# Performance work log

Measured on AMD Instinct MI355X. Metric: run time of the kernel, lower is better.

## Reference

```python
import jax, jax.numpy as jnp
import numpy as np

P, Q = 5, 4
C_IN, C_OUT = 256, 256


def setup_inputs() -> dict:
    key = jax.random.key(0)
    kx, kwp, kbp, kwq = jax.random.split(key, 4)
    x = jax.random.normal(kx, (32, C_IN, 56, 56), dtype=jnp.float32)
    # 1x1 conv weights: convp_i -> Wp[i-1] of shape [O, C]; only convp_1 has bias.
    Wp = jax.random.normal(kwp, (P, C_OUT, C_IN), dtype=jnp.float32) * (1.0 / np.sqrt(C_IN))
    bp = jax.random.normal(kbp, (C_OUT,), dtype=jnp.float32) * 0.01
    Wq = jax.random.normal(kwq, (Q, C_OUT, C_IN), dtype=jnp.float32) * (1.0 / np.sqrt(C_IN))
    return {"x": x, "Wp": Wp, "bp": bp, "Wq": Wq}


def reference(x, Wp, bp, Wq):
    # Build powers x**1 .. x**max(P,Q) via incremental multiply (same math as x**i).
    pmax = max(P, Q)
    pows = [x]
    for _ in range(pmax - 1):
        pows.append(pows[-1] * x)
    Xs = jnp.stack(pows, axis=0)  # [pmax, B, C, H, W]
    # Each 1x1 conv is a pointwise channel-mixing GEMM; sum over orders p/q.
    sum_p = jnp.einsum('pbchw,poc->bohw', Xs[:P], Wp) + bp[None, :, None, None]
    sum_q = jnp.einsum('qbchw,qoc->bohw', Xs[:Q], Wq)
    return sum_p / (1.0 + jnp.abs(sum_q))
```

## Files before the change

### kernel.cpp

```cpp
#include <hip/hip_runtime.h>


typedef __attribute__((ext_vector_type(8))) short bf16x8;
typedef __attribute__((ext_vector_type(4))) float f32x4;

#define CIN    256
#define HW3    3136
#define MTOT   100352
#define KTOT   1280
#define WPLANE (512 * 1280)

__device__ __forceinline__ unsigned short f2bf(float f) {
    union { float f; unsigned int u; } cv; cv.f = f;
    unsigned int u = cv.u;
    return (unsigned short)((u + 0x7FFFu + ((u >> 16) & 1u)) >> 16);
}
__device__ __forceinline__ float bf2f(unsigned short h) {
    union { unsigned int u; float f; } cv; cv.u = ((unsigned int)h) << 16;
    return cv.f;
}

__global__ void pack_w_kernel(const float* __restrict__ Wp,
                              const float* __restrict__ Wq,
                              unsigned short* __restrict__ Whi,
                              unsigned short* __restrict__ Wlo) {
    int idx = blockIdx.x * 256 + threadIdx.x;
    int n = idx / KTOT;
    int k = idx - n * KTOT;
    int p = k >> 8, c = k & 255;
    int o = ((n >> 5) << 4) + (n & 15);
    int isq = (n >> 4) & 1;
    float v;
    if (isq) v = (p < 4) ? Wq[((size_t)p * 256 + o) * 256 + c] : 0.0f;
    else     v = Wp[((size_t)p * 256 + o) * 256 + c];
    unsigned short h = f2bf(v);
    Whi[idx] = h;
    Wlo[idx] = f2bf(v - bf2f(h));
}

__device__ __forceinline__ bf16x8 pack_hi8(const float* v) {
    const unsigned int* u = (const unsigned int*)v;
    union { unsigned int w[4]; bf16x8 h; } r;
    r.w[0] = __builtin_amdgcn_perm(u[1], u[0], 0x07060302);
    r.w[1] = __builtin_amdgcn_perm(u[3], u[2], 0x07060302);
    r.w[2] = __builtin_amdgcn_perm(u[5], u[4], 0x07060302);
    r.w[3] = __builtin_amdgcn_perm(u[7], u[6], 0x07060302);
    return r.h;
}
__device__ __forceinline__ void resid8(const float* v, float* l) {
#pragma unroll
    for (int j = 0; j < 8; ++j) {
        union { unsigned int u; float f; } cv;
        cv.u = ((const unsigned int*)v)[j] & 0xFFFF0000u;
        l[j] = v[j] - cv.f;
    }
}

__global__ __launch_bounds__(256, 2) void kanv_gemm(
    const float* __restrict__ x,
    const unsigned short* __restrict__ Whi,
    const unsigned short* __restrict__ Wlo,
    const float* __restrict__ bp,
    float* __restrict__ out)
{
    __shared__ __align__(16) char sB[8 * 8192];

    const int tid  = threadIdx.x;
    const int lane = tid & 63;
    const int wave = tid >> 6;
    const int wm   = wave >> 1;
    const int wn   = wave & 1;
    const int col  = lane & 15;
    const int quad = lane >> 4;

    const int nt = blockIdx.x & 3;
    const int mt = blockIdx.x >> 2;
    const int m0 = mt * 128 + wm * 64;

    const float* xb[4];
#pragma unroll
    for (int mi = 0; mi < 4; ++mi) {
        int m  = m0 + mi * 16 + col;
        int bb = m / HW3, hw = m - bb * HW3;
        xb[mi] = x + ((size_t)bb * CIN) * HW3 + hw;
    }
    const unsigned short* wl4[2];
#pragma unroll
    for (int e = 0; e < 2; ++e) {
        int n = nt * 128 + wn * 64 + (2 * e) * 16 + col;
        wl4[e] = Wlo + (size_t)n * KTOT + quad * 8 + 4 * 256;
    }

    int voff[2];
#pragma unroll
    for (int ii = 0; ii < 2; ++ii) {
        int i = wave + 4 * ii;
        int n = i * 16 + col;
        voff[ii] = (nt * 128 + n) * 2560 + quad * 16;
    }
    const int rbase = (wn * 4) * 1024 + quad * 256 + col * 16;

    f32x4 acc[4][4];
#pragma unroll
    for (int mi = 0; mi < 4; ++mi)
#pragma unroll
        for (int ni = 0; ni < 4; ++ni)
            acc[mi][ni] = (f32x4){0.f, 0.f, 0.f, 0.f};

    float xv[4][8], pw[4][8], xn[4][8];

#pragma unroll
    for (int mi = 0; mi < 4; ++mi) {
        const float* xp = xb[mi] + (size_t)(quad * 8) * HW3;
#pragma unroll
        for (int j = 0; j < 8; ++j) { xv[mi][j] = xp[(size_t)j * HW3]; pw[mi][j] = xv[mi][j]; }
    }

    for (int g = 0; g < 8; ++g) {
        __syncthreads();

#pragma unroll
        for (int s = 0; s < 8; ++s) {
            const unsigned short* plane = (s < 5) ? Whi : Wlo;
            const int p = (s < 5) ? s : (s - 4);
            const char* srcb = (const char*)plane + (size_t)((p * 256 + g * 32) * 2);
#pragma unroll
            for (int ii = 0; ii < 2; ++ii) {
                const int i = wave + 4 * ii;
                __builtin_amdgcn_global_load_lds(
                    (const __attribute__((address_space(1))) void*)(srcb + voff[ii]),
                    (__attribute__((address_space(3))) void*)(sB + s * 8192 + i * 1024),
                    16, 0, 0);
            }
        }
        __syncthreads();

        if (g < 7) {
#pragma unroll
            for (int mi = 0; mi < 4; ++mi) {
                const float* xp = xb[mi] + (size_t)((g + 1) * 32 + quad * 8) * HW3;
#pragma unroll
                for (int j = 0; j < 8; ++j) xn[mi][j] = xp[(size_t)j * HW3];
            }
        }

#pragma unroll
        for (int p = 0; p < 5; ++p) {
            bf16x8 ah[4], al[4];
#pragma unroll
            for (int mi = 0; mi < 4; ++mi) {
                ah[mi] = pack_hi8(pw[mi]);
                if (p > 0) {
                    float lo[8];
                    resid8(pw[mi], lo);
                    al[mi] = pack_hi8(lo);
                }
            }
            const char* sb_p = sB + p * 8192 + rbase;
#pragma unroll
            for (int ni = 0; ni < 4; ++ni) {
                if (p == 4 && (ni & 1)) continue;
                bf16x8 bh = *(const bf16x8*)(sb_p + ni * 1024);
#pragma unroll
                for (int mi = 0; mi < 4; ++mi)
                    acc[mi][ni] = __builtin_amdgcn_mfma_f32_16x16x32_bf16(ah[mi], bh, acc[mi][ni], 0, 0, 0);
                if (p > 0) {
                    bf16x8 bl;
                    if (p < 4) bl = *(const bf16x8*)(sB + (p + 4) * 8192 + rbase + ni * 1024);
                    else       bl = *(const bf16x8*)(wl4[ni >> 1] + g * 32);
#pragma unroll
                    for (int mi = 0; mi < 4; ++mi) {
                        acc[mi][ni] = __builtin_amdgcn_mfma_f32_16x16x32_bf16(al[mi], bh, acc[mi][ni], 0, 0, 0);
                        acc[mi][ni] = __builtin_amdgcn_mfma_f32_16x16x32_bf16(ah[mi], bl, acc[mi][ni], 0, 0, 0);
                    }
                }
            }
            if (p < 4) {
#pragma unroll
                for (int mi = 0; mi < 4; ++mi)
#pragma unroll
                    for (int j = 0; j < 8; ++j) pw[mi][j] *= xv[mi][j];
            }
        }

        if (g < 7) {
#pragma unroll
            for (int mi = 0; mi < 4; ++mi)
#pragma unroll
                for (int j = 0; j < 8; ++j) { xv[mi][j] = xn[mi][j]; pw[mi][j] = xn[mi][j]; }
        }
    }

#pragma unroll
    for (int j = 0; j < 2; ++j) {
        const int o = (nt * 4 + wn * 2 + j) * 16 + col;
        const float bias = bp[o];
#pragma unroll
        for (int mi = 0; mi < 4; ++mi) {
            f32x4 sp = acc[mi][2 * j];
            f32x4 sq = acc[mi][2 * j + 1];
            const int mrow = m0 + mi * 16 + quad * 4;
            const int b2  = mrow / HW3;
            const int hw2 = mrow - b2 * HW3;
            float4 v;
            v.x = (sp[0] + bias) / (1.0f + fabsf(sq[0]));
            v.y = (sp[1] + bias) / (1.0f + fabsf(sq[1]));
            v.z = (sp[2] + bias) / (1.0f + fabsf(sq[2]));
            v.w = (sp[3] + bias) / (1.0f + fabsf(sq[3]));
            *(float4*)&out[((size_t)b2 * 256 + o) * HW3 + hw2] = v;
        }
    }
}

extern "C" void kernel_launch(void* const* d_in, const int* in_sizes, int n_in,
                              void* d_out, int out_size, void* d_ws, size_t ws_size,
                              hipStream_t stream) {
    const float* x  = (const float*)d_in[0];
    const float* Wp = (const float*)d_in[1];
    const float* bp = (const float*)d_in[2];
    const float* Wq = (const float*)d_in[3];
    float* out = (float*)d_out;
    unsigned short* Whi = (unsigned short*)d_ws;
    unsigned short* Wlo = Whi + WPLANE;

    pack_w_kernel<<<WPLANE / 256, 256, 0, stream>>>(Wp, Wq, Whi, Wlo);
    kanv_gemm<<<(MTOT / 128) * 4, 256, 0, stream>>>(x, Whi, Wlo, bp, out);
}
```

Before: 498.3 us.

## Halve block N-tile, shrink per-wave M-tile, remap blocks, raise occupancy

Each block now covers 64 output columns instead of 128, and each wave covers 32 rows with the full 64-column N tile, so accumulators and x registers are halved. The p=4 low-weight plane now goes to LDS instead of being read straight from global, and launch bounds ask for 3 blocks per CU. Block IDs are remapped so that blocks sharing an M tile are spread apart in launch order. The smaller tile means x powers and their hi/lo split are recomputed twice as often across blocks, which adds global x traffic and VALU work in exchange for lower register pressure and more occupancy.

```diff
diff --git a/kernel.cpp b/kernel.cpp
--- a/kernel.cpp
+++ b/kernel.cpp
@@ -56,61 +56,50 @@
     }
 }
 
-__global__ __launch_bounds__(256, 2) void kanv_gemm(
+__global__ __launch_bounds__(256, 3) void kanv_gemm(
     const float* __restrict__ x,
     const unsigned short* __restrict__ Whi,
     const unsigned short* __restrict__ Wlo,
     const float* __restrict__ bp,
     float* __restrict__ out)
 {
-    __shared__ __align__(16) char sB[8 * 8192];
+    __shared__ __align__(16) char sB[9 * 4096];
 
     const int tid  = threadIdx.x;
     const int lane = tid & 63;
     const int wave = tid >> 6;
-    const int wm   = wave >> 1;
-    const int wn   = wave & 1;
     const int col  = lane & 15;
     const int quad = lane >> 4;
 
-    const int nt = blockIdx.x & 3;
-    const int mt = blockIdx.x >> 2;
-    const int m0 = mt * 128 + wm * 64;
-
-    const float* xb[4];
-#pragma unroll
-    for (int mi = 0; mi < 4; ++mi) {
+    const int bid  = blockIdx.x;
+    const int orig = (bid & 7) * 784 + (bid >> 3);
+    const int nt = orig & 7;
+    const int mt = orig >> 3;
+    const int m0 = mt * 128 + wave * 32;
+
+    const float* xb[2];
+#pragma unroll
+    for (int mi = 0; mi < 2; ++mi) {
         int m  = m0 + mi * 16 + col;
         int bb = m / HW3, hw = m - bb * HW3;
         xb[mi] = x + ((size_t)bb * CIN) * HW3 + hw;
     }
-    const unsigned short* wl4[2];
-#pragma unroll
-    for (int e = 0; e < 2; ++e) {
-        int n = nt * 128 + wn * 64 + (2 * e) * 16 + col;
-        wl4[e] = Wlo + (size_t)n * KTOT + quad * 8 + 4 * 256;
-    }
-
-    int voff[2];
-#pragma unroll
-    for (int ii = 0; ii < 2; ++ii) {
-        int i = wave + 4 * ii;
-        int n = i * 16 + col;
-        voff[ii] = (nt * 128 + n) * 2560 + quad * 16;
-    }
-    const int rbase = (wn * 4) * 1024 + quad * 256 + col * 16;
-
-    f32x4 acc[4][4];
-#pragma unroll
-    for (int mi = 0; mi < 4; ++mi)
+
+    const int voff = (nt * 64 + wave * 16 + col) * 2560 + quad * 16;
+
+    const int rbase = quad * 256 + col * 16;
+
+    f32x4 acc[2][4];
+#pragma unroll
+    for (int mi = 0; mi < 2; ++mi)
 #pragma unroll
         for (int ni = 0; ni < 4; ++ni)
             acc[mi][ni] = (f32x4){0.f, 0.f, 0.f, 0.f};
 
-    float xv[4][8], pw[4][8], xn[4][8];
-
-#pragma unroll
-    for (int mi = 0; mi < 4; ++mi) {
+    float xv[2][8], pw[2][8], xn[2][8];
+
+#pragma unroll
+    for (int mi = 0; mi < 2; ++mi) {
         const float* xp = xb[mi] + (size_t)(quad * 8) * HW3;
 #pragma unroll
         for (int j = 0; j < 8; ++j) { xv[mi][j] = xp[(size_t)j * HW3]; pw[mi][j] = xv[mi][j]; }
@@ -120,24 +109,20 @@
         __syncthreads();
 
 #pragma unroll
-        for (int s = 0; s < 8; ++s) {
+        for (int s = 0; s < 9; ++s) {
             const unsigned short* plane = (s < 5) ? Whi : Wlo;
             const int p = (s < 5) ? s : (s - 4);
             const char* srcb = (const char*)plane + (size_t)((p * 256 + g * 32) * 2);
-#pragma unroll
-            for (int ii = 0; ii < 2; ++ii) {
-                const int i = wave + 4 * ii;
-                __builtin_amdgcn_global_load_lds(
-                    (const __attribute__((address_space(1))) void*)(srcb + voff[ii]),
-                    (__attribute__((address_space(3))) void*)(sB + s * 8192 + i * 1024),
-                    16, 0, 0);
-            }
+            __builtin_amdgcn_global_load_lds(
+                (const __attribute__((address_space(1))) void*)(srcb + voff),
+                (__attribute__((address_space(3))) void*)(sB + s * 4096 + wave * 1024),
+                16, 0, 0);
         }
         __syncthreads();
 
         if (g < 7) {
 #pragma unroll
-            for (int mi = 0; mi < 4; ++mi) {
+            for (int mi = 0; mi < 2; ++mi) {
                 const float* xp = xb[mi] + (size_t)((g + 1) * 32 + quad * 8) * HW3;
 #pragma unroll
                 for (int j = 0; j < 8; ++j) xn[mi][j] = xp[(size_t)j * HW3];
@@ -146,9 +131,9 @@
 
 #pragma unroll
         for (int p = 0; p < 5; ++p) {
-            bf16x8 ah[4], al[4];
-#pragma unroll
-            for (int mi = 0; mi < 4; ++mi) {
+            bf16x8 ah[2], al[2];
+#pragma unroll
+            for (int mi = 0; mi < 2; ++mi) {
                 ah[mi] = pack_hi8(pw[mi]);
                 if (p > 0) {
                     float lo[8];
@@ -156,20 +141,18 @@
                     al[mi] = pack_hi8(lo);
                 }
             }
-            const char* sb_p = sB + p * 8192 + rbase;
+            const char* sb_p = sB + p * 4096 + rbase;
 #pragma unroll
             for (int ni = 0; ni < 4; ++ni) {
                 if (p == 4 && (ni & 1)) continue;
                 bf16x8 bh = *(const bf16x8*)(sb_p + ni * 1024);
 #pragma unroll
-                for (int mi = 0; mi < 4; ++mi)
+                for (int mi = 0; mi < 2; ++mi)
                     acc[mi][ni] = __builtin_amdgcn_mfma_f32_16x16x32_bf16(ah[mi], bh, acc[mi][ni], 0, 0, 0);
                 if (p > 0) {
-                    bf16x8 bl;
-                    if (p < 4) bl = *(const bf16x8*)(sB + (p + 4) * 8192 + rbase + ni * 1024);
-                    else       bl = *(const bf16x8*)(wl4[ni >> 1] + g * 32);
-#pragma unroll
-                    for (int mi = 0; mi < 4; ++mi) {
+                    bf16x8 bl = *(const bf16x8*)(sB + (p + 4) * 4096 + rbase + ni * 1024);
+#pragma unroll
+                    for (int mi = 0; mi < 2; ++mi) {
                         acc[mi][ni] = __builtin_amdgcn_mfma_f32_16x16x32_bf16(al[mi], bh, acc[mi][ni], 0, 0, 0);
                         acc[mi][ni] = __builtin_amdgcn_mfma_f32_16x16x32_bf16(ah[mi], bl, acc[mi][ni], 0, 0, 0);
                     }
@@ -177,7 +160,7 @@
             }
             if (p < 4) {
 #pragma unroll
-                for (int mi = 0; mi < 4; ++mi)
+                for (int mi = 0; mi < 2; ++mi)
 #pragma unroll
                     for (int j = 0; j < 8; ++j) pw[mi][j] *= xv[mi][j];
             }
@@ -185,7 +168,7 @@
 
         if (g < 7) {
 #pragma unroll
-            for (int mi = 0; mi < 4; ++mi)
+            for (int mi = 0; mi < 2; ++mi)
 #pragma unroll
                 for (int j = 0; j < 8; ++j) { xv[mi][j] = xn[mi][j]; pw[mi][j] = xn[mi][j]; }
         }
@@ -193,10 +176,10 @@
 
 #pragma unroll
     for (int j = 0; j < 2; ++j) {
-        const int o = (nt * 4 + wn * 2 + j) * 16 + col;
+        const int o = (nt * 2 + j) * 16 + col;
         const float bias = bp[o];
 #pragma unroll
-        for (int mi = 0; mi < 4; ++mi) {
+        for (int mi = 0; mi < 2; ++mi) {
             f32x4 sp = acc[mi][2 * j];
             f32x4 sq = acc[mi][2 * j + 1];
             const int mrow = m0 + mi * 16 + quad * 4;
@@ -224,5 +207,5 @@
     unsigned short* Wlo = Whi + WPLANE;
 
     pack_w_kernel<<<WPLANE / 256, 256, 0, stream>>>(Wp, Wq, Whi, Wlo);
-    kanv_gemm<<<(MTOT / 128) * 4, 256, 0, stream>>>(x, Whi, Wlo, bp, out);
-}
+    kanv_gemm<<<(MTOT / 128) * 8, 256, 0, stream>>>(x, Whi, Wlo, bp, out);
+}
```

Measured after the change: 466.8 us. -6.3%, faster.
